# Kernel tuning notes

Measured on AMD Instinct MI355X. Metric: run time of the kernel, lower is better.

The kernel has to match this reference:

```python
import jax, jax.numpy as jnp
import numpy as np

IMG_H = 256; IMG_W = 256; N_PTS = 192
MIN_DEPTH = 3.0; MAX_DEPTH = 9.0
NDC_EXTENT = 1.0; FOCAL = 4.0  # focal length so rays at volume center span ~[-1,1]
EPS = 1e-8; EA_EPS = 1e-10


def setup_inputs() -> dict:
    key = jax.random.key(0)
    image3d = jax.random.uniform(key, (1, 1, 128, 128, 128), dtype=jnp.float32)
    R = jnp.eye(3, dtype=jnp.float32)[None]            # [1,3,3] camera rotation
    T = jnp.array([[0.0, 0.0, 4.0]], dtype=jnp.float32)  # camera center at world (0,0,-4)
    return {"image3d": image3d, "R": R, "T": T}


def _trilinear(vol, pts):
    # vol: [C,D,H,W]; pts: [N,3] xyz in [-1,1]; align_corners=True, zero padding
    C, D, H, W = vol.shape
    fx = (pts[:, 0] + 1.0) * 0.5 * (W - 1)
    fy = (pts[:, 1] + 1.0) * 0.5 * (H - 1)
    fz = (pts[:, 2] + 1.0) * 0.5 * (D - 1)
    x0 = jnp.floor(fx); y0 = jnp.floor(fy); z0 = jnp.floor(fz)
    wx = fx - x0; wy = fy - y0; wz = fz - z0
    out = jnp.zeros((pts.shape[0], C), vol.dtype)
    for dz in (0, 1):
        for dy in (0, 1):
            for dx in (0, 1):
                xi = x0 + dx; yi = y0 + dy; zi = z0 + dz
                w = ((wx if dx else 1.0 - wx) * (wy if dy else 1.0 - wy)
                     * (wz if dz else 1.0 - wz))
                valid = ((xi >= 0) & (xi <= W - 1) & (yi >= 0) & (yi <= H - 1)
                         & (zi >= 0) & (zi <= D - 1))
                xc = jnp.clip(xi, 0, W - 1).astype(jnp.int32)
                yc = jnp.clip(yi, 0, H - 1).astype(jnp.int32)
                zc = jnp.clip(zi, 0, D - 1).astype(jnp.int32)
                vals = vol[:, zc, yc, xc]          # [C,N] gather
                out = out + (w * valid).astype(vol.dtype)[:, None] * vals.T
    return out                                      # [N,C]


def reference(image3d, R, T):
    B = image3d.shape[0]
    features = jnp.repeat(image3d, 3, axis=1)                 # [B,3,D,H,W]
    densities = jnp.ones_like(image3d) / N_PTS                # [B,1,D,H,W]
    vol4 = jnp.concatenate([features, densities], axis=1)     # [B,4,D,H,W]
    # NDC pixel grid + depths along each ray
    ys = jnp.linspace(1.0, -1.0, IMG_H)
    xs = jnp.linspace(1.0, -1.0, IMG_W)
    yg, xg = jnp.meshgrid(ys, xs, indexing="ij")              # [H,W]
    depths = jnp.linspace(MIN_DEPTH, MAX_DEPTH, N_PTS)        # [P]
    x_cam = xg[..., None] * depths / FOCAL                    # [H,W,P]
    y_cam = yg[..., None] * depths / FOCAL
    z_cam = jnp.broadcast_to(depths, x_cam.shape)
    pts_cam = jnp.stack([x_cam, y_cam, z_cam], axis=-1)       # [H,W,P,3]
    # X_cam = X_world @ R + T  =>  X_world = (X_cam - T) @ R^T
    pts_world = jnp.einsum("bhwpj,bij->bhwpi",
                           pts_cam[None] - T[:, None, None, None, :], R)
    local = pts_world / NDC_EXTENT                            # volume local coords in [-1,1]
    sampled = jax.vmap(_trilinear)(vol4, local.reshape(B, -1, 3))  # [B,N,4]
    sampled = sampled.reshape(B, IMG_H, IMG_W, N_PTS, 4)
    feats = sampled[..., :3]
    dens = sampled[..., 3]                                    # [B,H,W,P]
    # EmissionAbsorption raymarcher (shifted cumprod of transmittance)
    t = (1.0 + EA_EPS) - dens
    cp = jnp.cumprod(t, axis=-1)
    absorption = jnp.concatenate([jnp.ones_like(cp[..., :1]), cp[..., :-1]], axis=-1)
    weights = dens * absorption
    rgb = jnp.einsum("bhwp,bhwpc->bhwc", weights, feats)      # [B,H,W,3]
    opac = 1.0 - jnp.prod(1.0 - dens, axis=-1, keepdims=True)
    rgba = jnp.concatenate([rgb, opac], axis=-1)              # [B,H,W,4]
    screen = jnp.transpose(rgba, (0, 3, 1, 2))                # [B,4,H,W]
    gray = screen.mean(axis=1, keepdims=True)                 # [B,1,H,W]
    # normalized(standardized(x))  (torch std is unbiased -> ddof=1)
    std = (gray - gray.mean()) / (jnp.std(gray, ddof=1) + EPS)
    out = (std - std.min() + EPS) / (std.max() - std.min() + EPS)
    return out
```

## Files before the change

kernel.cpp:

```cpp
#include <hip/hip_runtime.h>
#include <math.h>

#define N_PIX (256 * 256)
#define N_PTS 192
#define SEGS 8
#define TILE_PIX 64
#define N_BLK (N_PIX / TILE_PIX)
#define THREADS (TILE_PIX * SEGS)
#define VOL4_ELEMS (128 * 128 * 128)

__global__ __launch_bounds__(256) void pack_kernel(
    const float* __restrict__ vol, float4* __restrict__ vol4)
{
    const int idx = blockIdx.x * 256 + threadIdx.x;
    const int x = idx & 127;
    const int y = (idx >> 7) & 127;
    const int z = idx >> 14;
    const int x1 = min(x + 1, 127);
    const float* row0 = vol + (z * 128 + y) * 128;
    const float* row1 = vol + (z * 128 + min(y + 1, 127)) * 128;
    vol4[idx] = make_float4(row0[x], row0[x1], row1[x], row1[x1]);
}

__global__ __launch_bounds__(THREADS) void render_kernel(
    const float4* __restrict__ vol4,
    const float* __restrict__ Rm,
    const float* __restrict__ Tv,
    float* __restrict__ out,
    float* __restrict__ part)
{
    const int tid = threadIdx.x;
    const int seg = tid >> 6;
    const int l   = tid & 63;
    const int tr  = blockIdx.x >> 5;
    const int tc  = blockIdx.x & 31;
    const int h = tr * 8 + (l >> 3);
    const int w = tc * 8 + (l & 7);
    const float yg = 1.0f - (2.0f / 255.0f) * (float)h;
    const float xg = 1.0f - (2.0f / 255.0f) * (float)w;

    const float r00 = Rm[0], r01 = Rm[1], r02 = Rm[2];
    const float r10 = Rm[3], r11 = Rm[4], r12 = Rm[5];
    const float r20 = Rm[6], r21 = Rm[7], r22 = Rm[8];
    const float t0 = Tv[0], t1 = Tv[1], t2 = Tv[2];

    const float a0 = 0.25f * (r00 * xg + r01 * yg) + r02;
    const float a1 = 0.25f * (r10 * xg + r11 * yg) + r12;
    const float a2 = 0.25f * (r20 * xg + r21 * yg) + r22;
    const float b0 = -(r00 * t0 + r01 * t1 + r02 * t2);
    const float b1 = -(r10 * t0 + r11 * t1 + r12 * t2);
    const float b2 = -(r20 * t0 + r21 * t1 + r22 * t2);

    const float LIM = 1.0f + 2.0f / 127.0f + 1e-4f;
    float dlo = 3.0f, dhi = 9.0f;
    {
        const float aa[3] = {a0, a1, a2};
        const float bb[3] = {b0, b1, b2};
        #pragma unroll
        for (int k = 0; k < 3; ++k) {
            const float a = aa[k], b = bb[k];
            if (fabsf(a) > 1e-12f) {
                const float i0 = (-LIM - b) / a;
                const float i1 = ( LIM - b) / a;
                dlo = fmaxf(dlo, fminf(i0, i1));
                dhi = fminf(dhi, fmaxf(i0, i1));
            } else if (fabsf(b) >= LIM) {
                dhi = -1e30f;
            }
        }
    }
    const float step = 6.0f / 191.0f;
    const float rstep = 191.0f / 6.0f;
    int plo = (int)ceilf((dlo - 3.0f) * rstep - 1e-3f);
    int phi = (int)floorf((dhi - 3.0f) * rstep + 1e-3f);
    plo = max(plo, 0);
    phi = min(phi, N_PTS - 1);
    int len = phi - plo + 1;
    if (len < 0) len = 0;
    const int chunk = (len + SEGS - 1) >> 3;
    const int iBeg = plo + seg * chunk;
    const int iEnd = min(iBeg + chunk, plo + len);

    float P = 1.0f;
    float U = 1.0f;
    float S = 0.0f;

    #pragma unroll 2
    for (int p = iBeg; p < iEnd; ++p) {
        const float d = fmaf(step, (float)p, 3.0f);
        const float fx = (fmaf(a0, d, b0) + 1.0f) * 63.5f;
        const float fy = (fmaf(a1, d, b1) + 1.0f) * 63.5f;
        const float fz = (fmaf(a2, d, b2) + 1.0f) * 63.5f;
        const float x0f = floorf(fx), y0f = floorf(fy), z0f = floorf(fz);
        const float wx = fx - x0f, wy = fy - y0f, wz = fz - z0f;
        const int ix = (int)x0f, iy = (int)y0f, iz = (int)z0f;
        const float ax0 = (ix >= 0  && ix <= 127) ? (1.0f - wx) : 0.0f;
        const float ax1 = (ix >= -1 && ix <= 126) ? wx : 0.0f;
        const float ay0 = (iy >= 0  && iy <= 127) ? (1.0f - wy) : 0.0f;
        const float ay1 = (iy >= -1 && iy <= 126) ? wy : 0.0f;
        const float az0 = (iz >= 0  && iz <= 127) ? (1.0f - wz) : 0.0f;
        const float az1 = (iz >= -1 && iz <= 126) ? wz : 0.0f;
        const float s = (ax0 + ax1) * (ay0 + ay1) * (az0 + az1);
        const float dens = s * (1.0f / 192.0f);

        int xi = ix; float wx0 = ax0, wx1 = ax1;
        if (xi < 0) { xi = 0; wx0 = ax1; wx1 = 0.0f; } else { xi = min(xi, 127); }
        int yi = iy; float wy0 = ay0, wy1 = ay1;
        if (yi < 0) { yi = 0; wy0 = ay1; wy1 = 0.0f; } else { yi = min(yi, 127); }
        const int zc0 = min(max(iz, 0), 127);
        const int zc1 = min(max(iz + 1, 0), 127);

        const float4 c0 = vol4[(zc0 * 128 + yi) * 128 + xi];
        const float4 c1 = vol4[(zc1 * 128 + yi) * 128 + xi];
        const float bil0 = wy0 * (wx0 * c0.x + wx1 * c0.y)
                         + wy1 * (wx0 * c0.z + wx1 * c0.w);
        const float bil1 = wy0 * (wx0 * c1.x + wx1 * c1.y)
                         + wy1 * (wx0 * c1.z + wx1 * c1.w);
        const float feat = az0 * bil0 + az1 * bil1;

        S = fmaf(dens * P, feat, S);
        P *= (1.0f + 1e-10f - dens);
        U *= (1.0f - dens);
    }

    __shared__ float sP[SEGS][TILE_PIX];
    __shared__ float sU[SEGS][TILE_PIX];
    __shared__ float sS[SEGS][TILE_PIX];
    sP[seg][l] = P;
    sU[seg][l] = U;
    sS[seg][l] = S;
    __syncthreads();

    if (tid < TILE_PIX) {
        float absorb = 1.0f, uAll = 1.0f, wS = 0.0f;
        #pragma unroll
        for (int s = 0; s < SEGS; ++s) {
            wS = fmaf(absorb, sS[s][l], wS);
            absorb *= sP[s][l];
            uAll   *= sU[s][l];
        }
        const float g = (3.0f * wS + (1.0f - uAll)) * 0.25f;
        out[h * 256 + w] = g;

        float vs = g, vq = g * g, vmn = g, vmx = g;
        #pragma unroll
        for (int off = 1; off < 64; off <<= 1) {
            vs += __shfl_xor(vs, off);
            vq += __shfl_xor(vq, off);
            vmn = fminf(vmn, __shfl_xor(vmn, off));
            vmx = fmaxf(vmx, __shfl_xor(vmx, off));
        }
        if (l == 0) {
            part[blockIdx.x]             = vs;
            part[N_BLK + blockIdx.x]     = vq;
            part[2 * N_BLK + blockIdx.x] = vmn;
            part[3 * N_BLK + blockIdx.x] = vmx;
        }
    }
}

__global__ __launch_bounds__(256) void finish_kernel(
    float* __restrict__ out,
    const float* __restrict__ part)
{
    const int tid = threadIdx.x;
    __shared__ float s_s[4], s_q[4], s_n[4], s_x[4];
    __shared__ float s_fin[4];

    float fs  = part[tid]               + part[tid + 256]
              + part[tid + 512]         + part[tid + 768];
    float fq  = part[N_BLK + tid]       + part[N_BLK + tid + 256]
              + part[N_BLK + tid + 512] + part[N_BLK + tid + 768];
    float fn  = fminf(fminf(part[2 * N_BLK + tid],       part[2 * N_BLK + tid + 256]),
                      fminf(part[2 * N_BLK + tid + 512], part[2 * N_BLK + tid + 768]));
    float fx2 = fmaxf(fmaxf(part[3 * N_BLK + tid],       part[3 * N_BLK + tid + 256]),
                      fmaxf(part[3 * N_BLK + tid + 512], part[3 * N_BLK + tid + 768]));
    #pragma unroll
    for (int off = 1; off < 64; off <<= 1) {
        fs += __shfl_xor(fs, off);
        fq += __shfl_xor(fq, off);
        fn  = fminf(fn,  __shfl_xor(fn, off));
        fx2 = fmaxf(fx2, __shfl_xor(fx2, off));
    }
    const int wave = tid >> 6;
    const int lane = tid & 63;
    if (lane == 0) { s_s[wave] = fs; s_q[wave] = fq; s_n[wave] = fn; s_x[wave] = fx2; }
    __syncthreads();
    if (tid == 0) {
        const float tsum = s_s[0] + s_s[1] + s_s[2] + s_s[3];
        const float tsq  = s_q[0] + s_q[1] + s_q[2] + s_q[3];
        const float tmn  = fminf(fminf(s_n[0], s_n[1]), fminf(s_n[2], s_n[3]));
        const float tmx  = fmaxf(fmaxf(s_x[0], s_x[1]), fmaxf(s_x[2], s_x[3]));
        const float N = (float)N_PIX;
        const float mean = tsum / N;
        float var = (tsq - N * mean * mean) / (N - 1.0f);
        if (var < 0.0f) var = 0.0f;
        const float denom = sqrtf(var) + 1e-8f;
        s_fin[0] = mean;
        s_fin[1] = denom;
        s_fin[2] = (tmn - mean) / denom;
        s_fin[3] = (tmx - mean) / denom;
    }
    __syncthreads();

    const float mean = s_fin[0];
    const float rdenom = 1.0f / s_fin[1];
    const float smin = s_fin[2];
    const float rrange = 1.0f / (s_fin[3] - smin + 1e-8f);
    const int i = blockIdx.x * 256 + tid;
    const float sv = (out[i] - mean) * rdenom;
    out[i] = (sv - smin + 1e-8f) * rrange;
}

extern "C" void kernel_launch(void* const* d_in, const int* in_sizes, int n_in,
                              void* d_out, int out_size, void* d_ws, size_t ws_size,
                              hipStream_t stream)
{
    const float* vol = (const float*)d_in[0];
    const float* Rm  = (const float*)d_in[1];
    const float* Tv  = (const float*)d_in[2];
    float* out = (float*)d_out;
    float4* vol4 = (float4*)d_ws;
    float* part = (float*)d_ws + 4 * VOL4_ELEMS;

    hipLaunchKernelGGL(pack_kernel, dim3(VOL4_ELEMS / 256), dim3(256), 0, stream,
                       vol, vol4);
    hipLaunchKernelGGL(render_kernel, dim3(N_BLK), dim3(THREADS), 0, stream,
                       vol4, Rm, Tv, out, part);
    hipLaunchKernelGGL(finish_kernel, dim3(N_PIX / 256), dim3(256), 0, stream,
                       out, part);
}
```

Baseline: 85.74 us.

## Pack full 2x2x2 trilinear corner neighborhood as fp16 into one 16-byte load

The pack kernel now stores all eight trilinear corners of each voxel as fp16 pairs in a single uint4, so the render loop issues one 16-byte gather per sample instead of two float4 gathers. The z-boundary case is handled like x and y by clamping and shifting the weights. The loop unroll factor is also raised from 2 to 4. The volume stays 16 bytes per voxel, and storing it in fp16 adds rounding error to the sampled features.

```diff
diff --git a/kernel.cpp b/kernel.cpp
--- a/kernel.cpp
+++ b/kernel.cpp
@@ -1,4 +1,5 @@
 #include <hip/hip_runtime.h>
+#include <hip/hip_fp16.h>
 #include <math.h>
 
 #define N_PIX (256 * 256)
@@ -7,23 +8,36 @@
 #define TILE_PIX 64
 #define N_BLK (N_PIX / TILE_PIX)
 #define THREADS (TILE_PIX * SEGS)
-#define VOL4_ELEMS (128 * 128 * 128)
+#define VOL_ELEMS (128 * 128 * 128)
 
 __global__ __launch_bounds__(256) void pack_kernel(
-    const float* __restrict__ vol, float4* __restrict__ vol4)
+    const float* __restrict__ vol, uint4* __restrict__ vol8)
 {
     const int idx = blockIdx.x * 256 + threadIdx.x;
     const int x = idx & 127;
     const int y = (idx >> 7) & 127;
     const int z = idx >> 14;
     const int x1 = min(x + 1, 127);
-    const float* row0 = vol + (z * 128 + y) * 128;
-    const float* row1 = vol + (z * 128 + min(y + 1, 127)) * 128;
-    vol4[idx] = make_float4(row0[x], row0[x1], row1[x], row1[x1]);
+    const int y1 = min(y + 1, 127);
+    const int z1 = min(z + 1, 127);
+    const float* p00 = vol + (z  * 128 + y ) * 128;
+    const float* p01 = vol + (z  * 128 + y1) * 128;
+    const float* p10 = vol + (z1 * 128 + y ) * 128;
+    const float* p11 = vol + (z1 * 128 + y1) * 128;
+    const __half2 h0 = __floats2half2_rn(p00[x], p00[x1]);
+    const __half2 h1 = __floats2half2_rn(p01[x], p01[x1]);
+    const __half2 h2 = __floats2half2_rn(p10[x], p10[x1]);
+    const __half2 h3 = __floats2half2_rn(p11[x], p11[x1]);
+    uint4 o;
+    o.x = *(const unsigned int*)&h0;
+    o.y = *(const unsigned int*)&h1;
+    o.z = *(const unsigned int*)&h2;
+    o.w = *(const unsigned int*)&h3;
+    vol8[idx] = o;
 }
 
 __global__ __launch_bounds__(THREADS) void render_kernel(
-    const float4* __restrict__ vol4,
+    const uint4* __restrict__ vol8,
     const float* __restrict__ Rm,
     const float* __restrict__ Tv,
     float* __restrict__ out,
@@ -85,7 +99,7 @@
     float U = 1.0f;
     float S = 0.0f;
 
-    #pragma unroll 2
+    #pragma unroll 4
     for (int p = iBeg; p < iEnd; ++p) {
         const float d = fmaf(step, (float)p, 3.0f);
         const float fx = (fmaf(a0, d, b0) + 1.0f) * 63.5f;
@@ -107,16 +121,19 @@
         if (xi < 0) { xi = 0; wx0 = ax1; wx1 = 0.0f; } else { xi = min(xi, 127); }
         int yi = iy; float wy0 = ay0, wy1 = ay1;
         if (yi < 0) { yi = 0; wy0 = ay1; wy1 = 0.0f; } else { yi = min(yi, 127); }
-        const int zc0 = min(max(iz, 0), 127);
-        const int zc1 = min(max(iz + 1, 0), 127);
-
-        const float4 c0 = vol4[(zc0 * 128 + yi) * 128 + xi];
-        const float4 c1 = vol4[(zc1 * 128 + yi) * 128 + xi];
-        const float bil0 = wy0 * (wx0 * c0.x + wx1 * c0.y)
-                         + wy1 * (wx0 * c0.z + wx1 * c0.w);
-        const float bil1 = wy0 * (wx0 * c1.x + wx1 * c1.y)
-                         + wy1 * (wx0 * c1.z + wx1 * c1.w);
-        const float feat = az0 * bil0 + az1 * bil1;
+        int zi = iz; float wz0 = az0, wz1 = az1;
+        if (zi < 0) { zi = 0; wz0 = az1; wz1 = 0.0f; } else { zi = min(zi, 127); }
+
+        const uint4 raw = vol8[(zi * 128 + yi) * 128 + xi];
+        const __half2 h0 = *(const __half2*)&raw.x;
+        const __half2 h1 = *(const __half2*)&raw.y;
+        const __half2 h2 = *(const __half2*)&raw.z;
+        const __half2 h3 = *(const __half2*)&raw.w;
+        const float bil0 = wy0 * fmaf(wx0, __low2float(h0), wx1 * __high2float(h0))
+                         + wy1 * fmaf(wx0, __low2float(h1), wx1 * __high2float(h1));
+        const float bil1 = wy0 * fmaf(wx0, __low2float(h2), wx1 * __high2float(h2))
+                         + wy1 * fmaf(wx0, __low2float(h3), wx1 * __high2float(h3));
+        const float feat = fmaf(wz0, bil0, wz1 * bil1);
 
         S = fmaf(dens * P, feat, S);
         P *= (1.0f + 1e-10f - dens);
@@ -220,13 +237,13 @@
     const float* Rm  = (const float*)d_in[1];
     const float* Tv  = (const float*)d_in[2];
     float* out = (float*)d_out;
-    float4* vol4 = (float4*)d_ws;
-    float* part = (float*)d_ws + 4 * VOL4_ELEMS;
-
-    hipLaunchKernelGGL(pack_kernel, dim3(VOL4_ELEMS / 256), dim3(256), 0, stream,
-                       vol, vol4);
+    uint4* vol8 = (uint4*)d_ws;
+    float* part = (float*)((char*)d_ws + VOL_ELEMS * 16);
+
+    hipLaunchKernelGGL(pack_kernel, dim3(VOL_ELEMS / 256), dim3(256), 0, stream,
+                       vol, (uint4*)d_ws);
     hipLaunchKernelGGL(render_kernel, dim3(N_BLK), dim3(THREADS), 0, stream,
-                       vol4, Rm, Tv, out, part);
+                       vol8, Rm, Tv, out, part);
     hipLaunchKernelGGL(finish_kernel, dim3(N_PIX / 256), dim3(256), 0, stream,
                        out, part);
 }
```

Result: no change. 85.75 us (+0.0%).
